# Performance work log

Hardware: AMD Instinct MI355X
Metric: run time of the kernel (lower is better)

## Reference

```python
import jax, jax.numpy as jnp
import numpy as np

N_NODES = 100000
HIDDEN = 128
IN_FEAT = 128
N_EDGES = 600000


def setup_inputs() -> dict:
    key = jax.random.key(0)
    ks = jax.random.split(key, 8)
    x = jax.random.normal(ks[0], (N_NODES, IN_FEAT), dtype=jnp.float32)
    edge_index = jax.random.randint(ks[1], (2, N_EDGES), 0, N_NODES, dtype=jnp.int64)
    # Glorot-style init for the three GCNConv layers (in->hidden, hidden->hidden, hidden->hidden)
    s_in = 1.0 / np.sqrt(IN_FEAT)
    s_h = 1.0 / np.sqrt(HIDDEN)
    W1 = jax.random.normal(ks[2], (IN_FEAT, HIDDEN), dtype=jnp.float32) * s_in
    b1 = jnp.zeros((HIDDEN,), dtype=jnp.float32)
    W2 = jax.random.normal(ks[3], (HIDDEN, HIDDEN), dtype=jnp.float32) * s_h
    b2 = jnp.zeros((HIDDEN,), dtype=jnp.float32)
    W3 = jax.random.normal(ks[4], (HIDDEN, HIDDEN), dtype=jnp.float32) * s_h
    b3 = jnp.zeros((HIDDEN,), dtype=jnp.float32)
    return {"x": x, "W1": W1, "b1": b1, "W2": W2, "b2": b2, "W3": W3, "b3": b3,
            "edge_index": edge_index}


def _gcn_conv(x, W, b, row, col, norm, n_nodes):
    # GCNConv (add_self_loops=False): out = D^{-1/2} A D^{-1/2} (x W) + b
    h = x @ W                                   # [N, H]
    msg = h[row] * norm[:, None]                # gather sources, scale per edge [E, H]
    agg = jax.ops.segment_sum(msg, col, num_segments=n_nodes)  # scatter-add to targets
    return agg + b


def reference(x, W1, b1, W2, b2, W3, b3, edge_index):
    row, col = edge_index[0], edge_index[1]
    # Symmetric GCN normalization, no self loops, unit edge weights.
    deg = jax.ops.segment_sum(jnp.ones(row.shape[0], dtype=x.dtype), col,
                              num_segments=N_NODES)
    deg_inv_sqrt = jnp.where(deg > 0, jax.lax.rsqrt(jnp.maximum(deg, 1.0)), 0.0)
    norm = deg_inv_sqrt[row] * deg_inv_sqrt[col]  # [E]

    h = _gcn_conv(x, W1, b1, row, col, norm, N_NODES)
    h = jax.nn.relu(h)  # dropout(p=0.1) is identity in eval mode
    h = _gcn_conv(h, W2, b2, row, col, norm, N_NODES)
    h = jax.nn.relu(h)
    h = _gcn_conv(h, W3, b3, row, col, norm, N_NODES)
    return h
```

## Files before the change

### kernel.cpp

```cpp
#include <hip/hip_runtime.h>
#include <cstddef>

#define NN 100000
#define NE 600000
#define HID 128

typedef _Float16 half8 __attribute__((ext_vector_type(8)));
typedef _Float16 half2v __attribute__((ext_vector_type(2)));
typedef float f32x4 __attribute__((ext_vector_type(4)));

union H8 { _Float16 h[8]; half2v p[4]; uint4 u; half8 v; };

__global__ void k_degi(const int* __restrict__ col, int* __restrict__ degi, int E) {
    int e = blockIdx.x * blockDim.x + threadIdx.x;
    if (e < E) atomicAdd(&degi[col[e]], 1);
}

__global__ void k_wprep(const float* __restrict__ W1, const float* __restrict__ W2,
                        const float* __restrict__ W3, _Float16* __restrict__ wt) {
    int b = blockIdx.x;
    int layer = b >> 7, k = b & 127;
    const float* W = layer == 0 ? W1 : (layer == 1 ? W2 : W3);
    int c = threadIdx.x;
    wt[((size_t)layer << 14) + c * 128 + k] = (_Float16)W[k * 128 + c];
}

__global__ void k_blocksum(const int* __restrict__ degi, float* __restrict__ dinv,
                           int* __restrict__ bsum, int N) {
    __shared__ int sh[256];
    int i = blockIdx.x * 256 + threadIdx.x;
    int v = i < N ? degi[i] : 0;
    if (i < N) dinv[i] = v > 0 ? rsqrtf((float)v) : 0.0f;
    sh[threadIdx.x] = v;
    __syncthreads();
    for (int s = 128; s > 0; s >>= 1) {
        if (threadIdx.x < s) sh[threadIdx.x] += sh[threadIdx.x + s];
        __syncthreads();
    }
    if (threadIdx.x == 0) bsum[blockIdx.x] = sh[0];
}

__global__ void k_scan_bsum(int* __restrict__ bsum, int nb) {
    __shared__ int sh[512];
    int tid = threadIdx.x;
    int v = (tid < nb) ? bsum[tid] : 0;
    sh[tid] = v;
    __syncthreads();
    #pragma unroll
    for (int s = 1; s < 512; s <<= 1) {
        int t = (tid >= s) ? sh[tid - s] : 0;
        __syncthreads();
        sh[tid] += t;
        __syncthreads();
    }
    if (tid < nb) bsum[tid] = sh[tid] - v;
}

__global__ void k_scan_apply(const int* __restrict__ degi, const int* __restrict__ bsum,
                             int* __restrict__ rowptr, int* __restrict__ cursor, int N) {
    __shared__ int sh[256];
    int i = blockIdx.x * 256 + threadIdx.x;
    int v = (i < N) ? degi[i] : 0;
    sh[threadIdx.x] = v;
    __syncthreads();
    #pragma unroll
    for (int s = 1; s < 256; s <<= 1) {
        int t = (threadIdx.x >= s) ? sh[threadIdx.x - s] : 0;
        __syncthreads();
        sh[threadIdx.x] += t;
        __syncthreads();
    }
    if (i < N) {
        int excl = bsum[blockIdx.x] + sh[threadIdx.x] - v;
        rowptr[i] = excl;
        cursor[i] = excl;
        if (i == N - 1) rowptr[N] = bsum[blockIdx.x] + sh[threadIdx.x];
    }
}

__global__ void k_fill_csr(const int* __restrict__ row, const int* __restrict__ col,
                           int* __restrict__ cursor, int* __restrict__ csr_off, int E) {
    int e = blockIdx.x * blockDim.x + threadIdx.x;
    if (e >= E) return;
    int r = row[e], c = col[e];
    int pos = atomicAdd(&cursor[c], 1);
    csr_off[pos] = r * (HID * 2);
}

template <typename TA>
__global__ __launch_bounds__(256, 2) void k_gemm(
    const TA* __restrict__ A, const _Float16* __restrict__ WT,
    const float* __restrict__ dinv, _Float16* __restrict__ H, int nrows)
{
    __shared__ _Float16 asl[128 * 128];
    __shared__ _Float16 wsl[128 * 128];
    const int tid  = threadIdx.x;
    const int lane = tid & 63;
    const int w    = tid >> 6;
    const int wm   = w >> 1, wn = w & 1;
    const int ln15 = lane & 15;
    const int hi   = lane >> 4;
    const int row0 = blockIdx.x * 128;

    #pragma unroll
    for (int i = 0; i < 8; ++i) {
        int g = i * 256 + tid;
        int c = g >> 4, k8 = (g & 15) << 3;
        uint4 wv = *(const uint4*)(WT + c * 128 + k8);
        *(uint4*)&wsl[c * 128 + (k8 ^ ((c & 7) << 3))] = wv;
    }
    #pragma unroll
    for (int i = 0; i < 8; ++i) {
        int g = i * 256 + tid;
        int r = g >> 4, c8 = (g & 15) << 3;
        int gr = row0 + r; if (gr >= nrows) gr = nrows - 1;
        if constexpr (sizeof(TA) == 4) {
            const float4* src = (const float4*)(A + (size_t)gr * HID + c8);
            float4 v0 = src[0], v1 = src[1];
            H8 o;
            o.h[0] = (_Float16)v0.x; o.h[1] = (_Float16)v0.y;
            o.h[2] = (_Float16)v0.z; o.h[3] = (_Float16)v0.w;
            o.h[4] = (_Float16)v1.x; o.h[5] = (_Float16)v1.y;
            o.h[6] = (_Float16)v1.z; o.h[7] = (_Float16)v1.w;
            *(uint4*)&asl[r * 128 + (c8 ^ ((r & 7) << 3))] = o.u;
        } else {
            uint4 u = *(const uint4*)(A + (size_t)gr * HID + c8);
            *(uint4*)&asl[r * 128 + (c8 ^ ((r & 7) << 3))] = u;
        }
    }
    __syncthreads();

    f32x4 acc[4][4];
    #pragma unroll
    for (int i = 0; i < 4; ++i)
        #pragma unroll
        for (int j = 0; j < 4; ++j) {
            acc[i][j][0] = 0.0f; acc[i][j][1] = 0.0f;
            acc[i][j][2] = 0.0f; acc[i][j][3] = 0.0f;
        }

    #pragma unroll
    for (int ks = 0; ks < 4; ++ks) {
        const int k0 = ks * 32 + hi * 8;
        half8 a[4], b[4];
        #pragma unroll
        for (int i = 0; i < 4; ++i) {
            int ra = wm * 64 + i * 16 + ln15;
            a[i] = *(const half8*)&asl[ra * 128 + (k0 ^ ((ra & 7) << 3))];
            int cb = wn * 64 + i * 16 + ln15;
            b[i] = *(const half8*)&wsl[cb * 128 + (k0 ^ ((cb & 7) << 3))];
        }
        #pragma unroll
        for (int i = 0; i < 4; ++i)
            #pragma unroll
            for (int j = 0; j < 4; ++j)
                acc[i][j] = __builtin_amdgcn_mfma_f32_16x16x32_f16(a[i], b[j], acc[i][j], 0, 0, 0);
    }

    #pragma unroll
    for (int i = 0; i < 4; ++i) {
        #pragma unroll
        for (int q = 0; q < 4; ++q) {
            int r = row0 + wm * 64 + i * 16 + hi * 4 + q;
            if (r < nrows) {
                float s = dinv[r];
                #pragma unroll
                for (int j = 0; j < 4; ++j) {
                    H[(size_t)r * HID + wn * 64 + j * 16 + ln15] =
                        (_Float16)(acc[i][j][q] * s);
                }
            }
        }
    }
}

template <int MODE>
__global__ __launch_bounds__(256) void k_aggregate(
    const _Float16* __restrict__ hs, const int* __restrict__ csr_off,
    const int* __restrict__ rowptr, const float* __restrict__ dinv,
    const float* __restrict__ bias, void* __restrict__ aggv, int N)
{
    int node = blockIdx.x * 4 + (threadIdx.x >> 6);
    if (node >= N) return;
    int lane = threadIdx.x & 63;
    int es   = lane >> 4;
    int fg   = lane & 15;
    int beg = rowptr[node], end = rowptr[node + 1];

    float accf[8];
    #pragma unroll
    for (int j = 0; j < 8; ++j) accf[j] = 0.0f;

#if __has_builtin(__builtin_amdgcn_fdot2)
    const half2v selx = {(_Float16)1.0f, (_Float16)0.0f};
    const half2v sely = {(_Float16)0.0f, (_Float16)1.0f};
#define ACC8(hh)                                                              \
    do {                                                                      \
        _Pragma("unroll")                                                     \
        for (int p = 0; p < 4; ++p) {                                         \
            accf[2*p]   = __builtin_amdgcn_fdot2((hh).p[p], selx, accf[2*p],   false); \
            accf[2*p+1] = __builtin_amdgcn_fdot2((hh).p[p], sely, accf[2*p+1], false); \
        }                                                                     \
    } while (0)
#else
#define ACC8(hh)                                                              \
    do {                                                                      \
        _Pragma("unroll")                                                     \
        for (int j = 0; j < 8; ++j) accf[j] += (float)(hh).h[j];              \
    } while (0)
#endif

    const uint4 z = make_uint4(0, 0, 0, 0);
    const char* hb = (const char*)hs;
    int nr = (end - beg + 3) >> 2;
    int e  = beg + es;
    int r  = 0;
    for (; r + 1 < nr; r += 2, e += 8) {
        int o0 = (e     < end) ? csr_off[e]     : -1;
        int o1 = (e + 4 < end) ? csr_off[e + 4] : -1;
        uint4 u0 = (o0 >= 0) ? *(const uint4*)(hb + (size_t)(unsigned)o0 + fg * 16) : z;
        uint4 u1 = (o1 >= 0) ? *(const uint4*)(hb + (size_t)(unsigned)o1 + fg * 16) : z;
        H8 h0; h0.u = u0;
        H8 h1; h1.u = u1;
        ACC8(h0);
        ACC8(h1);
    }
    if (r < nr) {
        int o0 = (e < end) ? csr_off[e] : -1;
        uint4 u0 = (o0 >= 0) ? *(const uint4*)(hb + (size_t)(unsigned)o0 + fg * 16) : z;
        H8 h0; h0.u = u0;
        ACC8(h0);
    }
#undef ACC8

    #pragma unroll
    for (int j = 0; j < 8; ++j) {
        accf[j] += __shfl_xor(accf[j], 16);
        accf[j] += __shfl_xor(accf[j], 32);
    }

    float v0 = es < 2 ? (es == 0 ? accf[0] : accf[2])
                      : (es == 2 ? accf[4] : accf[6]);
    float v1 = es < 2 ? (es == 0 ? accf[1] : accf[3])
                      : (es == 2 ? accf[5] : accf[7]);
    int f0 = fg * 8 + es * 2;
    float s = dinv[node];
    float2 bv = *(const float2*)(bias + f0);
    v0 = v0 * s + bv.x;
    v1 = v1 * s + bv.y;
    if constexpr (MODE == 0) {
        union { _Float16 h[2]; unsigned u; } o;
        o.h[0] = (_Float16)fmaxf(v0, 0.0f);
        o.h[1] = (_Float16)fmaxf(v1, 0.0f);
        *(unsigned*)((_Float16*)aggv + (size_t)node * HID + f0) = o.u;
    } else {
        *(float2*)((float*)aggv + (size_t)node * HID + f0) = make_float2(v0, v1);
    }
}

extern "C" void kernel_launch(void* const* d_in, const int* in_sizes, int n_in,
                              void* d_out, int out_size, void* d_ws, size_t ws_size,
                              hipStream_t stream)
{
    const float* x  = (const float*)d_in[0];
    const float* W1 = (const float*)d_in[1];
    const float* b1 = (const float*)d_in[2];
    const float* W2 = (const float*)d_in[3];
    const float* b2 = (const float*)d_in[4];
    const float* W3 = (const float*)d_in[5];
    const float* b3 = (const float*)d_in[6];
    const int*   ei = (const int*)d_in[7];
    const int* row  = ei;
    const int* colv = ei + NE;
    float* out = (float*)d_out;

    _Float16* h16 = (_Float16*)d_ws;
    _Float16* a16 = h16 + (size_t)NN * HID;
    _Float16* wt  = a16 + (size_t)NN * HID;
    int*   degi    = (int*)(wt + 3 * 128 * 128);
    float* dinv    = (float*)(degi + NN);
    int*   rowptr  = (int*)(dinv + NN);
    int*   cursor  = rowptr + NN + 1;
    int*   bsum    = cursor + NN;
    int*   csr_off = bsum + 512;

    const int TB = 256;
    const int nScanBlocks = (NN + 255) / 256;

    k_wprep<<<384, 128, 0, stream>>>(W1, W2, W3, wt);
    hipMemsetAsync(degi, 0, NN * sizeof(int), stream);
    k_degi      <<<(NE + TB - 1) / TB, TB, 0, stream>>>(colv, degi, NE);
    k_blocksum  <<<nScanBlocks, 256, 0, stream>>>(degi, dinv, bsum, NN);
    k_scan_bsum <<<1, 512, 0, stream>>>(bsum, nScanBlocks);
    k_scan_apply<<<nScanBlocks, 256, 0, stream>>>(degi, bsum, rowptr, cursor, NN);
    k_fill_csr  <<<(NE + TB - 1) / TB, TB, 0, stream>>>(row, colv, cursor, csr_off, NE);

    const int gemmBlocks = (NN + 127) / 128;
    const int aggBlocks  = (NN + 3) / 4;

    k_gemm<float><<<gemmBlocks, TB, 0, stream>>>(x, wt, dinv, h16, NN);
    k_aggregate<0><<<aggBlocks, TB, 0, stream>>>(h16, csr_off, rowptr, dinv, b1, a16, NN);
    k_gemm<_Float16><<<gemmBlocks, TB, 0, stream>>>(a16, wt + (1 << 14), dinv, h16, NN);
    k_aggregate<0><<<aggBlocks, TB, 0, stream>>>(h16, csr_off, rowptr, dinv, b2, a16, NN);
    k_gemm<_Float16><<<gemmBlocks, TB, 0, stream>>>(a16, wt + (2 << 14), dinv, h16, NN);
    k_aggregate<1><<<aggBlocks, TB, 0, stream>>>(h16, csr_off, rowptr, dinv, b3, out, NN);
}
```

Baseline: 253.7 us.

## Batch 32 nodes per aggregate block and stage CSR offsets in LDS

The aggregation kernel now gives each block 32 consecutive nodes instead of 4, with each wave looping over 8 nodes. The block first loads the 33 row pointers into shared memory, then copies the block's contiguous CSR offset range into an LDS buffer when it fits in 2048 entries, falling back to global memory otherwise. The intent is to cut per-block launch and rowptr overhead and to read neighbour offsets from LDS. In exchange it adds two barriers, serializes nodes within a wave (less memory-level parallelism per wave), and launches fewer blocks.

```diff
diff --git a/kernel.cpp b/kernel.cpp
--- a/kernel.cpp
+++ b/kernel.cpp
@@ -180,16 +180,31 @@
     const int* __restrict__ rowptr, const float* __restrict__ dinv,
     const float* __restrict__ bias, void* __restrict__ aggv, int N)
 {
-    int node = blockIdx.x * 4 + (threadIdx.x >> 6);
-    if (node >= N) return;
-    int lane = threadIdx.x & 63;
-    int es   = lane >> 4;
-    int fg   = lane & 15;
-    int beg = rowptr[node], end = rowptr[node + 1];
-
-    float accf[8];
-    #pragma unroll
-    for (int j = 0; j < 8; ++j) accf[j] = 0.0f;
+    constexpr int NB = 32;
+    constexpr int CAP = 2048;
+    __shared__ int s_off[CAP + 8];
+    __shared__ int s_ptr[NB + 1];
+
+    const int tid = threadIdx.x;
+    const int n0  = blockIdx.x * NB;
+    if (tid <= NB) s_ptr[tid] = rowptr[n0 + tid];
+    __syncthreads();
+    const int Rbeg = s_ptr[0];
+    const int cnt  = s_ptr[NB] - Rbeg;
+    const bool fast = cnt <= CAP;
+    if (fast) {
+        for (int i = tid; i < cnt; i += 256) s_off[i] = csr_off[Rbeg + i];
+    }
+    __syncthreads();
+    const int* offp = fast ? (const int*)s_off : (csr_off + Rbeg);
+
+    const int lane = tid & 63;
+    const int w    = tid >> 6;
+    const int es   = lane >> 4;
+    const int fg   = lane & 15;
+    const char* hb = (const char*)hs;
+    const int f0   = fg * 8 + es * 2;
+    const float2 bv = *(const float2*)(bias + f0);
 
 #if __has_builtin(__builtin_amdgcn_fdot2)
     const half2v selx = {(_Float16)1.0f, (_Float16)0.0f};
@@ -210,52 +225,61 @@
     } while (0)
 #endif
 
-    const uint4 z = make_uint4(0, 0, 0, 0);
-    const char* hb = (const char*)hs;
-    int nr = (end - beg + 3) >> 2;
-    int e  = beg + es;
-    int r  = 0;
-    for (; r + 1 < nr; r += 2, e += 8) {
-        int o0 = (e     < end) ? csr_off[e]     : -1;
-        int o1 = (e + 4 < end) ? csr_off[e + 4] : -1;
-        uint4 u0 = (o0 >= 0) ? *(const uint4*)(hb + (size_t)(unsigned)o0 + fg * 16) : z;
-        uint4 u1 = (o1 >= 0) ? *(const uint4*)(hb + (size_t)(unsigned)o1 + fg * 16) : z;
-        H8 h0; h0.u = u0;
-        H8 h1; h1.u = u1;
-        ACC8(h0);
-        ACC8(h1);
-    }
-    if (r < nr) {
-        int o0 = (e < end) ? csr_off[e] : -1;
-        uint4 u0 = (o0 >= 0) ? *(const uint4*)(hb + (size_t)(unsigned)o0 + fg * 16) : z;
-        H8 h0; h0.u = u0;
-        ACC8(h0);
+    #pragma unroll 2
+    for (int t = 0; t < 8; ++t) {
+        const int ni   = (w << 3) + t;
+        const int node = n0 + ni;
+        const int beg  = s_ptr[ni] - Rbeg;
+        const int end  = s_ptr[ni + 1] - Rbeg;
+
+        float accf[8];
+        #pragma unroll
+        for (int j = 0; j < 8; ++j) accf[j] = 0.0f;
+
+        const uint4 z = make_uint4(0, 0, 0, 0);
+        int nr  = (end - beg + 3) >> 2;
+        int idx = beg + es;
+        int r   = 0;
+        for (; r + 1 < nr; r += 2, idx += 8) {
+            int o0 = (idx     < end) ? offp[idx]     : -1;
+            int o1 = (idx + 4 < end) ? offp[idx + 4] : -1;
+            uint4 u0 = (o0 >= 0) ? *(const uint4*)(hb + (size_t)(unsigned)o0 + fg * 16) : z;
+            uint4 u1 = (o1 >= 0) ? *(const uint4*)(hb + (size_t)(unsigned)o1 + fg * 16) : z;
+            H8 h0; h0.u = u0;
+            H8 h1; h1.u = u1;
+            ACC8(h0);
+            ACC8(h1);
+        }
+        if (r < nr) {
+            int o0 = (idx < end) ? offp[idx] : -1;
+            uint4 u0 = (o0 >= 0) ? *(const uint4*)(hb + (size_t)(unsigned)o0 + fg * 16) : z;
+            H8 h0; h0.u = u0;
+            ACC8(h0);
+        }
+
+        #pragma unroll
+        for (int j = 0; j < 8; ++j) {
+            accf[j] += __shfl_xor(accf[j], 16);
+            accf[j] += __shfl_xor(accf[j], 32);
+        }
+
+        float v0 = es < 2 ? (es == 0 ? accf[0] : accf[2])
+                          : (es == 2 ? accf[4] : accf[6]);
+        float v1 = es < 2 ? (es == 0 ? accf[1] : accf[3])
+                          : (es == 2 ? accf[5] : accf[7]);
+        float s = dinv[node];
+        v0 = v0 * s + bv.x;
+        v1 = v1 * s + bv.y;
+        if constexpr (MODE == 0) {
+            union { _Float16 h[2]; unsigned u; } o;
+            o.h[0] = (_Float16)fmaxf(v0, 0.0f);
+            o.h[1] = (_Float16)fmaxf(v1, 0.0f);
+            *(unsigned*)((_Float16*)aggv + (size_t)node * HID + f0) = o.u;
+        } else {
+            *(float2*)((float*)aggv + (size_t)node * HID + f0) = make_float2(v0, v1);
+        }
     }
 #undef ACC8
-
-    #pragma unroll
-    for (int j = 0; j < 8; ++j) {
-        accf[j] += __shfl_xor(accf[j], 16);
-        accf[j] += __shfl_xor(accf[j], 32);
-    }
-
-    float v0 = es < 2 ? (es == 0 ? accf[0] : accf[2])
-                      : (es == 2 ? accf[4] : accf[6]);
-    float v1 = es < 2 ? (es == 0 ? accf[1] : accf[3])
-                      : (es == 2 ? accf[5] : accf[7]);
-    int f0 = fg * 8 + es * 2;
-    float s = dinv[node];
-    float2 bv = *(const float2*)(bias + f0);
-    v0 = v0 * s + bv.x;
-    v1 = v1 * s + bv.y;
-    if constexpr (MODE == 0) {
-        union { _Float16 h[2]; unsigned u; } o;
-        o.h[0] = (_Float16)fmaxf(v0, 0.0f);
-        o.h[1] = (_Float16)fmaxf(v1, 0.0f);
-        *(unsigned*)((_Float16*)aggv + (size_t)node * HID + f0) = o.u;
-    } else {
-        *(float2*)((float*)aggv + (size_t)node * HID + f0) = make_float2(v0, v1);
-    }
 }
 
 extern "C" void kernel_launch(void* const* d_in, const int* in_sizes, int n_in,
@@ -296,7 +320,7 @@
     k_fill_csr  <<<(NE + TB - 1) / TB, TB, 0, stream>>>(row, colv, cursor, csr_off, NE);
 
     const int gemmBlocks = (NN + 127) / 128;
-    const int aggBlocks  = (NN + 3) / 4;
+    const int aggBlocks  = (NN + 31) / 32;
 
     k_gemm<float><<<gemmBlocks, TB, 0, stream>>>(x, wt, dinv, h16, NN);
     k_aggregate<0><<<aggBlocks, TB, 0, stream>>>(h16, csr_off, rowptr, dinv, b1, a16, NN);
```

Result: faster. 247.9 us (-2.3%).
